# Kernel tuning notes

Measured on AMD Instinct MI355X. Metric: run time of the kernel, lower is better.

## Reference

```python
import jax, jax.numpy as jnp
import numpy as np

GRID_SIZE = 3
SPLINE_ORDER = 3

def make_grid():
    # grid_range=[-1,1], h=2/grid_size; extended grid of length grid_size+2k+1 = 10
    h = 2.0 / GRID_SIZE
    return (jnp.arange(-SPLINE_ORDER, GRID_SIZE + SPLINE_ORDER + 1, dtype=jnp.float32) * h - 1.0)

def b_splines(x, grid):
    # x: [N, F] -> bases [N, F, grid_size+spline_order]
    xg = x[..., None]
    bases = ((xg >= grid[:-1]) & (xg < grid[1:])).astype(x.dtype)
    for j in range(1, SPLINE_ORDER + 1):
        left = (xg - grid[: -(j + 1)]) / (grid[j:-1] - grid[: -(j + 1)])
        right = (grid[j + 1:] - xg) / (grid[j + 1:] - grid[1:-j])
        bases = left * bases[..., :-1] + right * bases[..., 1:]
    return bases

def kan_linear(x, base_w, spline_w, scaler, grid):
    # x: [N, F]; base_w: [O, F]; spline_w: [O, F, G]; scaler: [O, F]
    base = jax.nn.silu(x) @ base_w.T
    sb = b_splines(x, grid)                      # [N, F, G]
    spl = jnp.einsum('nfg,ofg->no', sb, spline_w * scaler[..., None])
    return base + spl

def kan_conv3x3(x, base_w, spline_w, scaler, grid):
    # x: [B, C, H, W]; 3x3 kernel, pad 1, stride 1 -> [B, O, H, W]
    B, C, H, W = x.shape
    patches = jax.lax.conv_general_dilated_patches(
        x, (3, 3), (1, 1), ((1, 1), (1, 1)))     # [B, C*9, H, W]
    p = patches.transpose(0, 2, 3, 1).reshape(B * H * W, C * 9)
    y = kan_linear(p, base_w, spline_w, scaler, grid)
    return y.reshape(B, H, W, -1).transpose(0, 3, 1, 2)

def maxpool2(x):
    return jax.lax.reduce_window(x, -jnp.inf, jax.lax.max,
                                 (1, 1, 2, 2), (1, 1, 2, 2), 'VALID')

def setup_inputs() -> dict:
    key = jax.random.key(0)
    ks = jax.random.split(key, 12)
    s = 0.1
    return {
        'x': jax.random.normal(ks[0], (256, 3, 32, 32), jnp.float32),
        'c1_base_w': jax.random.normal(ks[1], (8, 27), jnp.float32) * s,
        'c1_spline_w': jax.random.normal(ks[2], (8, 27, 6), jnp.float32) * s,
        'c1_scaler': jax.random.normal(ks[3], (8, 27), jnp.float32) * s,
        'c2_base_w': jax.random.normal(ks[4], (16, 72), jnp.float32) * s,
        'c2_spline_w': jax.random.normal(ks[5], (16, 72, 6), jnp.float32) * s,
        'c2_scaler': jax.random.normal(ks[6], (16, 72), jnp.float32) * s,
        'c3_base_w': jax.random.normal(ks[7], (32, 144), jnp.float32) * s,
        'c3_spline_w': jax.random.normal(ks[8], (32, 144, 6), jnp.float32) * s,
        'c3_scaler': jax.random.normal(ks[9], (32, 144), jnp.float32) * s,
        'lin_w': jax.random.normal(ks[10], (100, 512), jnp.float32) * s,
        'lin_b': jax.random.normal(ks[11], (100,), jnp.float32) * s,
    }

def reference(x, c1_base_w, c1_spline_w, c1_scaler,
              c2_base_w, c2_spline_w, c2_scaler,
              c3_base_w, c3_spline_w, c3_scaler,
              lin_w, lin_b):
    grid = make_grid()
    h = maxpool2(kan_conv3x3(x, c1_base_w, c1_spline_w, c1_scaler, grid))   # [B,8,16,16]
    h = maxpool2(kan_conv3x3(h, c2_base_w, c2_spline_w, c2_scaler, grid))   # [B,16,8,8]
    h = maxpool2(kan_conv3x3(h, c3_base_w, c3_spline_w, c3_scaler, grid))   # [B,32,4,4]
    h = h.reshape(h.shape[0], -1)                                           # [B,512]
    return h @ lin_w.T + lin_b                                              # [B,100]
```

## Files before the change

kernel.cpp:

```cpp
#include <hip/hip_runtime.h>
#include <hip/hip_bf16.h>
#include <math.h>


#define BATCH 256

typedef short bf16x8 __attribute__((ext_vector_type(8)));
typedef float f32x4  __attribute__((ext_vector_type(4)));

__device__ __forceinline__ unsigned pk2(float a, float b) {
    __hip_bfloat162 h = __float22bfloat162_rn(make_float2(a, b));
    unsigned u;
    __builtin_memcpy(&u, &h, 4);
    return u;
}
__device__ __forceinline__ unsigned f2bf(float f) {
    __hip_bfloat16 h = __float2bfloat16(f);
    unsigned short us;
    __builtin_memcpy(&us, &h, 2);
    return (unsigned)us;
}

__device__ __forceinline__ void bspline_basis(float x, float bs[6]) {
    float s  = (x + 3.0f) * 1.5f;
    float cf = floorf(s);
    float t  = s - cf;
    int  ci  = (int)cf;
    float t2 = t * t, t3 = t2 * t;
    float omt = 1.0f - t;
    const float k6 = 1.0f / 6.0f;
    float w0 = omt * omt * omt * k6;
    float w1 = (3.0f * t3 - 6.0f * t2 + 4.0f) * k6;
    float w2 = (-3.0f * t3 + 3.0f * t2 + 3.0f * t + 1.0f) * k6;
    float w3 = t3 * k6;
#pragma unroll
    for (int i = 0; i < 6; ++i) {
        int j = i - ci + 3;
        float v = 0.0f;
        v = (j == 0) ? w0 : v;
        v = (j == 1) ? w1 : v;
        v = (j == 2) ? w2 : v;
        v = (j == 3) ? w3 : v;
        bs[i] = v;
    }
}

__device__ __forceinline__ uint4 act_record(float val) {
    float silu = __fdividef(val, 1.0f + __expf(-val));
    float bs[6];
    bspline_basis(val, bs);
    uint4 r;
    r.x = pk2(silu, bs[0]);
    r.y = pk2(bs[1], bs[2]);
    r.z = pk2(bs[3], bs[4]);
    r.w = f2bf(bs[5]);
    return r;
}

__device__ __forceinline__ uint4 fuse_w(const float* bw, const float* sw,
                                        const float* sc, int j) {
    float s = sc[j];
    uint4 r;
    r.x = pk2(bw[j],             sw[j * 6 + 0] * s);
    r.y = pk2(sw[j * 6 + 1] * s, sw[j * 6 + 2] * s);
    r.z = pk2(sw[j * 6 + 3] * s, sw[j * 6 + 4] * s);
    r.w = f2bf(sw[j * 6 + 5] * s);
    return r;
}

__global__ __launch_bounds__(512, 4) void kan_l1(
        const float* __restrict__ x,
        const float* __restrict__ bw, const float* __restrict__ sw,
        const float* __restrict__ sc,
        const float* __restrict__ bw3, const float* __restrict__ sw3,
        const float* __restrict__ sc3,
        uint4* __restrict__ w3g,
        float* __restrict__ out) {
    constexpr int C = 3, F = 27, FP = 28, NS = 7;
    constexpr int RT = 18, TC = 34, NT = 512;

    __shared__ uint4 s_act[C * RT * TC];
    __shared__ uint4 s_w[FP * 16];

    const int tid = threadIdx.x;
    const int bid = blockIdx.x;
    const int b   = bid >> 1;
    const int v   = bid & 1;

    if (bid < 9) {
        int i = bid * NT + tid;
        if (i < 4608) {
            int o = i / 144, fp = i % 144;
            w3g[fp * 32 + o] = fuse_w(bw3, sw3, sc3, i);
        }
    }

    for (int i = tid; i < FP * 16; i += NT) {
        int fp = i >> 4, o = i & 15;
        uint4 r = make_uint4(0u, 0u, 0u, 0u);
        if (fp < F && o < 8) r = fuse_w(bw, sw, sc, o * F + fp);
        s_w[i] = r;
    }

    const uint4 zrec = act_record(0.0f);
    for (int i = tid; i < C * RT * TC; i += NT) s_act[i] = zrec;
    __syncthreads();
    const float* xb = x + (size_t)b * C * 32 * 32;
    if (tid < 408) {
        int cc  = tid / 136;
        int rem = tid - cc * 136;
        int rr_i = rem >> 3;
        int c4   = (rem & 7) * 4;
        float4 v4 = *(const float4*)&xb[(cc * 32 + rr_i + 15 * v) * 32 + c4];
        uint4* dst = &s_act[(cc * RT + rr_i + 1 - v) * TC + c4 + 1];
        dst[0] = act_record(v4.x);
        dst[1] = act_record(v4.y);
        dst[2] = act_record(v4.z);
        dst[3] = act_record(v4.w);
    }
    __syncthreads();

    const int lane = tid & 63;
    const int wv   = tid >> 6;
    const int kg   = lane >> 4;
    const int oc   = lane & 15;
    const int m    = lane & 15;

    bf16x8 bfr[NS];
#pragma unroll
    for (int s = 0; s < NS; ++s)
        bfr[s] = *reinterpret_cast<const bf16x8*>(&s_w[(4 * s + kg) * 16 + oc]);

    int pixoff[4];
#pragma unroll
    for (int t = 0; t < 4; ++t)
        pixoff[t] = (2 * wv + (t >> 1)) * TC + 16 * (t & 1) + m;

    f32x4 acc[4];
#pragma unroll
    for (int t = 0; t < 4; ++t) acc[t] = (f32x4){0.f, 0.f, 0.f, 0.f};

#pragma unroll
    for (int s = 0; s < NS; ++s) {
        int tp = 4 * s + kg;
        tp = (tp > F - 1) ? F - 1 : tp;
        int c  = tp / 9;
        int t9 = tp - 9 * c;
        int ky = t9 / 3;
        int kx = t9 - 3 * ky;
        int base = (c * RT + ky) * TC + kx;
#pragma unroll
        for (int t = 0; t < 4; ++t) {
            bf16x8 a = *reinterpret_cast<const bf16x8*>(&s_act[base + pixoff[t]]);
            acc[t] = __builtin_amdgcn_mfma_f32_16x16x32_bf16(a, bfr[s], acc[t], 0, 0, 0);
        }
    }

    if (oc < 8) {
        f32x4 e0, e1;
#pragma unroll
        for (int p = 0; p < 4; ++p) {
            e0[p] = fmaxf(acc[0][p], acc[2][p]);
            e1[p] = fmaxf(acc[1][p], acc[3][p]);
        }
        float* op = out + (((size_t)b * 8 + oc) * 16 + (8 * v + wv)) * 16;
        op[2 * kg]         = fmaxf(e0[0], e0[1]);
        op[2 * kg + 1]     = fmaxf(e0[2], e0[3]);
        op[8 + 2 * kg]     = fmaxf(e1[0], e1[1]);
        op[8 + 2 * kg + 1] = fmaxf(e1[2], e1[3]);
    }
}

__global__ __launch_bounds__(512, 2) void kan_l2l3lin(
        const float* __restrict__ h1,
        const float* __restrict__ bw2, const float* __restrict__ sw2,
        const float* __restrict__ sc2,
        const uint4* __restrict__ w3g,
        const float* __restrict__ lin_w, const float* __restrict__ lin_b,
        float* __restrict__ out) {
    constexpr int NT = 512;
    __shared__ alignas(16) unsigned char s_mem[59904];
    uint4* s_act2 = (uint4*)s_mem;
    uint4* s_w2   = (uint4*)(s_mem + 41472);
    float* s_h2   = (float*)s_mem;
    uint4* s_act3 = (uint4*)(s_mem + 4096);
    float* s_h3   = (float*)s_mem;

    const int tid = threadIdx.x;
    const int n   = blockIdx.x;
    const int lane = tid & 63;
    const int wv   = tid >> 6;
    const int kg   = lane >> 4;
    const int oc   = lane & 15;
    const int m    = lane & 15;

    const uint4 zrec = act_record(0.0f);

    for (int i = tid; i < 72 * 16; i += NT) {
        int fp = i >> 4, o = i & 15;
        s_w2[i] = fuse_w(bw2, sw2, sc2, o * 72 + fp);
    }
    for (int i = tid; i < 2592; i += NT) s_act2[i] = zrec;
    __syncthreads();
    {
        const float4* xb4 = (const float4*)(h1 + (size_t)n * 8 * 16 * 16);
        float4 v4 = xb4[tid];
        int cc   = tid >> 6;
        int rr_i = (tid >> 2) & 15;
        int c4   = (tid & 3) * 4;
        uint4* dst = &s_act2[(cc * 18 + rr_i + 1) * 18 + c4 + 1];
        dst[0] = act_record(v4.x);
        dst[1] = act_record(v4.y);
        dst[2] = act_record(v4.z);
        dst[3] = act_record(v4.w);
    }
    __syncthreads();

    {
        bf16x8 bfr2[18];
#pragma unroll
        for (int s = 0; s < 18; ++s)
            bfr2[s] = *reinterpret_cast<const bf16x8*>(&s_w2[(4 * s + kg) * 16 + oc]);
        const int p0 = (2 * wv) * 18 + m;
        const int p1 = p0 + 18;
        f32x4 a0 = (f32x4){0.f, 0.f, 0.f, 0.f}, a1 = a0, b0 = a0, b1 = a0;
#pragma unroll
        for (int s = 0; s < 18; ++s) {
            int tp = 4 * s + kg;
            int c  = tp / 9;
            int t9 = tp - 9 * c;
            int ky = t9 / 3;
            int kx = t9 - 3 * ky;
            int base = (c * 18 + ky) * 18 + kx;
            bf16x8 av0 = *reinterpret_cast<const bf16x8*>(&s_act2[base + p0]);
            bf16x8 av1 = *reinterpret_cast<const bf16x8*>(&s_act2[base + p1]);
            if (s < 9) {
                a0 = __builtin_amdgcn_mfma_f32_16x16x32_bf16(av0, bfr2[s], a0, 0, 0, 0);
                a1 = __builtin_amdgcn_mfma_f32_16x16x32_bf16(av1, bfr2[s], a1, 0, 0, 0);
            } else {
                b0 = __builtin_amdgcn_mfma_f32_16x16x32_bf16(av0, bfr2[s], b0, 0, 0, 0);
                b1 = __builtin_amdgcn_mfma_f32_16x16x32_bf16(av1, bfr2[s], b1, 0, 0, 0);
            }
        }
        a0 = a0 + b0;
        a1 = a1 + b1;
        float e0 = fmaxf(a0[0], a1[0]);
        float e1 = fmaxf(a0[1], a1[1]);
        float e2 = fmaxf(a0[2], a1[2]);
        float e3 = fmaxf(a0[3], a1[3]);
        __syncthreads();
        s_h2[(oc * 8 + wv) * 8 + 2 * kg]     = fmaxf(e0, e1);
        s_h2[(oc * 8 + wv) * 8 + 2 * kg + 1] = fmaxf(e2, e3);
    }
    __syncthreads();

    for (int i = tid; i < 1600; i += NT) s_act3[i] = zrec;
    __syncthreads();
    for (int i = tid; i < 1024; i += NT) {
        float val = s_h2[i];
        int cc   = i >> 6;
        int rr_i = (i >> 3) & 7;
        int col_i = i & 7;
        s_act3[(cc * 10 + rr_i + 1) * 10 + col_i + 1] = act_record(val);
    }
    __syncthreads();

    {
        const int mt  = wv & 3;
        const int o03 = 16 * (wv >> 2);
        bf16x8 bfr3[36];
#pragma unroll
        for (int s = 0; s < 36; ++s)
            bfr3[s] = *reinterpret_cast<const bf16x8*>(&w3g[(4 * s + kg) * 32 + o03 + oc]);
        const int poff = (2 * mt + (m >> 3)) * 10 + (m & 7);
        f32x4 a3 = (f32x4){0.f, 0.f, 0.f, 0.f}, a3b = a3;
#pragma unroll
        for (int s = 0; s < 36; ++s) {
            int tp = 4 * s + kg;
            int c  = tp / 9;
            int t9 = tp - 9 * c;
            int ky = t9 / 3;
            int kx = t9 - 3 * ky;
            int base = (c * 10 + ky) * 10 + kx;
            bf16x8 av = *reinterpret_cast<const bf16x8*>(&s_act3[base + poff]);
            if (s < 18)
                a3 = __builtin_amdgcn_mfma_f32_16x16x32_bf16(av, bfr3[s], a3, 0, 0, 0);
            else
                a3b = __builtin_amdgcn_mfma_f32_16x16x32_bf16(av, bfr3[s], a3b, 0, 0, 0);
        }
        a3 = a3 + a3b;
        float q0 = fmaxf(a3[0], a3[1]);
        float q1 = fmaxf(a3[2], a3[3]);
        float y0 = fmaxf(q0, __shfl_xor(q0, 32));
        float y1 = fmaxf(q1, __shfl_xor(q1, 32));
        if (kg < 2) {
            s_h3[(o03 + oc) * 16 + mt * 4 + 2 * kg]     = y0;
            s_h3[(o03 + oc) * 16 + mt * 4 + 2 * kg + 1] = y1;
        }
    }
    __syncthreads();

    {
        const float4* hf = (const float4*)s_h3;
        const float4 h0v = hf[lane];
        const float4 h1v = hf[lane + 64];
        const float4* wr = (const float4*)(lin_w + (size_t)wv * 512);
        float4 w0 = wr[lane];
        float4 w1 = wr[lane + 64];
#pragma unroll 1
        for (int o = wv; o < 100; o += 8) {
            float4 nw0, nw1;
            const int on = o + 8;
            if (on < 100) {
                const float4* wn = (const float4*)(lin_w + (size_t)on * 512);
                nw0 = wn[lane];
                nw1 = wn[lane + 64];
            }
            float p = w0.x * h0v.x + w0.y * h0v.y + w0.z * h0v.z + w0.w * h0v.w
                    + w1.x * h1v.x + w1.y * h1v.y + w1.z * h1v.z + w1.w * h1v.w;
            p += __shfl_xor(p, 32);
            p += __shfl_xor(p, 16);
            p += __shfl_xor(p, 8);
            p += __shfl_xor(p, 4);
            p += __shfl_xor(p, 2);
            p += __shfl_xor(p, 1);
            if (lane == 0) out[(size_t)n * 100 + o] = p + lin_b[o];
            w0 = nw0;
            w1 = nw1;
        }
    }
}

extern "C" void kernel_launch(void* const* d_in, const int* in_sizes, int n_in,
                              void* d_out, int out_size, void* d_ws, size_t ws_size,
                              hipStream_t stream) {
    const float* x     = (const float*)d_in[0];
    const float* c1_bw = (const float*)d_in[1];
    const float* c1_sw = (const float*)d_in[2];
    const float* c1_sc = (const float*)d_in[3];
    const float* c2_bw = (const float*)d_in[4];
    const float* c2_sw = (const float*)d_in[5];
    const float* c2_sc = (const float*)d_in[6];
    const float* c3_bw = (const float*)d_in[7];
    const float* c3_sw = (const float*)d_in[8];
    const float* c3_sc = (const float*)d_in[9];
    const float* lin_w = (const float*)d_in[10];
    const float* lin_b = (const float*)d_in[11];
    float* out = (float*)d_out;

    float* ws = (float*)d_ws;
    float* h1 = ws;
    uint4* w3g = (uint4*)(h1 + 524288);

    kan_l1<<<512, 512, 0, stream>>>(x, c1_bw, c1_sw, c1_sc,
                                    c3_bw, c3_sw, c3_sc, w3g, h1);
    kan_l2l3lin<<<256, 512, 0, stream>>>(h1, c2_bw, c2_sw, c2_sc,
                                         w3g, lin_w, lin_b, out);
}
```

Baseline: 98.91 us.

## Store layer-1 output as precomputed spline records and prefuse layer-2 weights globally

Layer 1 now writes its pooled outputs as packed bf16 activation/B-spline records instead of fp32 values, and also fuses layer-2 weights into a global buffer. Layer 2 copies records straight into shared memory and loads both layer-2 and layer-3 weight fragments into registers up front. This removes per-block basis evaluation and weight fusion in the second kernel and shrinks its shared memory. The cost is a fourfold larger intermediate tensor in global memory and higher register pressure from the hoisted weights.

```diff
diff --git a/kernel.cpp b/kernel.cpp
--- a/kernel.cpp
+++ b/kernel.cpp
@@ -72,10 +72,12 @@
         const float* __restrict__ x,
         const float* __restrict__ bw, const float* __restrict__ sw,
         const float* __restrict__ sc,
+        const float* __restrict__ bw2, const float* __restrict__ sw2,
+        const float* __restrict__ sc2,
         const float* __restrict__ bw3, const float* __restrict__ sw3,
         const float* __restrict__ sc3,
-        uint4* __restrict__ w3g,
-        float* __restrict__ out) {
+        uint4* __restrict__ w2g, uint4* __restrict__ w3g,
+        uint4* __restrict__ grec) {
     constexpr int C = 3, F = 27, FP = 28, NS = 7;
     constexpr int RT = 18, TC = 34, NT = 512;
 
@@ -87,11 +89,17 @@
     const int b   = bid >> 1;
     const int v   = bid & 1;
 
-    if (bid < 9) {
+    if (bid < 12) {
         int i = bid * NT + tid;
-        if (i < 4608) {
-            int o = i / 144, fp = i % 144;
-            w3g[fp * 32 + o] = fuse_w(bw3, sw3, sc3, i);
+        if (i < 5760) {
+            if (i < 1152) {
+                int o = i / 72, fp = i % 72;
+                w2g[fp * 16 + o] = fuse_w(bw2, sw2, sc2, i);
+            } else {
+                int j = i - 1152;
+                int o = j / 144, fp = j % 144;
+                w3g[fp * 32 + o] = fuse_w(bw3, sw3, sc3, j);
+            }
         }
     }
 
@@ -163,25 +171,23 @@
             e0[p] = fmaxf(acc[0][p], acc[2][p]);
             e1[p] = fmaxf(acc[1][p], acc[3][p]);
         }
-        float* op = out + (((size_t)b * 8 + oc) * 16 + (8 * v + wv)) * 16;
-        op[2 * kg]         = fmaxf(e0[0], e0[1]);
-        op[2 * kg + 1]     = fmaxf(e0[2], e0[3]);
-        op[8 + 2 * kg]     = fmaxf(e1[0], e1[1]);
-        op[8 + 2 * kg + 1] = fmaxf(e1[2], e1[3]);
+        uint4* op = grec + (((size_t)b * 8 + oc) * 16 + (8 * v + wv)) * 16;
+        op[2 * kg]         = act_record(fmaxf(e0[0], e0[1]));
+        op[2 * kg + 1]     = act_record(fmaxf(e0[2], e0[3]));
+        op[8 + 2 * kg]     = act_record(fmaxf(e1[0], e1[1]));
+        op[8 + 2 * kg + 1] = act_record(fmaxf(e1[2], e1[3]));
     }
 }
 
 __global__ __launch_bounds__(512, 2) void kan_l2l3lin(
-        const float* __restrict__ h1,
-        const float* __restrict__ bw2, const float* __restrict__ sw2,
-        const float* __restrict__ sc2,
+        const uint4* __restrict__ grec,
+        const uint4* __restrict__ w2g,
         const uint4* __restrict__ w3g,
         const float* __restrict__ lin_w, const float* __restrict__ lin_b,
         float* __restrict__ out) {
     constexpr int NT = 512;
-    __shared__ alignas(16) unsigned char s_mem[59904];
+    __shared__ alignas(16) unsigned char s_mem[41472];
     uint4* s_act2 = (uint4*)s_mem;
-    uint4* s_w2   = (uint4*)(s_mem + 41472);
     float* s_h2   = (float*)s_mem;
     uint4* s_act3 = (uint4*)(s_mem + 4096);
     float* s_h3   = (float*)s_mem;
@@ -196,31 +202,31 @@
 
     const uint4 zrec = act_record(0.0f);
 
-    for (int i = tid; i < 72 * 16; i += NT) {
-        int fp = i >> 4, o = i & 15;
-        s_w2[i] = fuse_w(bw2, sw2, sc2, o * 72 + fp);
-    }
+    bf16x8 bfr2[18];
+#pragma unroll
+    for (int s = 0; s < 18; ++s)
+        bfr2[s] = *reinterpret_cast<const bf16x8*>(&w2g[(4 * s + kg) * 16 + oc]);
+    const int o03 = 16 * (wv >> 2);
+    bf16x8 bfr3[36];
+#pragma unroll
+    for (int s = 0; s < 36; ++s)
+        bfr3[s] = *reinterpret_cast<const bf16x8*>(&w3g[(4 * s + kg) * 32 + o03 + oc]);
+
     for (int i = tid; i < 2592; i += NT) s_act2[i] = zrec;
     __syncthreads();
     {
-        const float4* xb4 = (const float4*)(h1 + (size_t)n * 8 * 16 * 16);
-        float4 v4 = xb4[tid];
-        int cc   = tid >> 6;
-        int rr_i = (tid >> 2) & 15;
-        int c4   = (tid & 3) * 4;
-        uint4* dst = &s_act2[(cc * 18 + rr_i + 1) * 18 + c4 + 1];
-        dst[0] = act_record(v4.x);
-        dst[1] = act_record(v4.y);
-        dst[2] = act_record(v4.z);
-        dst[3] = act_record(v4.w);
+        const uint4* grn = grec + (size_t)n * 2048;
+#pragma unroll
+        for (int k = 0; k < 4; ++k) {
+            int i = tid + k * NT;
+            uint4 r = grn[i];
+            int cc = i >> 8, rr_i = (i >> 4) & 15, col = i & 15;
+            s_act2[(cc * 18 + rr_i + 1) * 18 + col + 1] = r;
+        }
     }
     __syncthreads();
 
     {
-        bf16x8 bfr2[18];
-#pragma unroll
-        for (int s = 0; s < 18; ++s)
-            bfr2[s] = *reinterpret_cast<const bf16x8*>(&s_w2[(4 * s + kg) * 16 + oc]);
         const int p0 = (2 * wv) * 18 + m;
         const int p1 = p0 + 18;
         f32x4 a0 = (f32x4){0.f, 0.f, 0.f, 0.f}, a1 = a0, b0 = a0, b1 = a0;
@@ -267,11 +273,6 @@
 
     {
         const int mt  = wv & 3;
-        const int o03 = 16 * (wv >> 2);
-        bf16x8 bfr3[36];
-#pragma unroll
-        for (int s = 0; s < 36; ++s)
-            bfr3[s] = *reinterpret_cast<const bf16x8*>(&w3g[(4 * s + kg) * 32 + o03 + oc]);
         const int poff = (2 * mt + (m >> 3)) * 10 + (m & 7);
         f32x4 a3 = (f32x4){0.f, 0.f, 0.f, 0.f}, a3b = a3;
 #pragma unroll
@@ -348,12 +349,12 @@
     const float* lin_b = (const float*)d_in[11];
     float* out = (float*)d_out;
 
-    float* ws = (float*)d_ws;
-    float* h1 = ws;
-    uint4* w3g = (uint4*)(h1 + 524288);
+    uint4* grec = (uint4*)d_ws;
+    uint4* w2g  = grec + 524288;
+    uint4* w3g  = w2g + 1152;
 
     kan_l1<<<512, 512, 0, stream>>>(x, c1_bw, c1_sw, c1_sc,
-                                    c3_bw, c3_sw, c3_sc, w3g, h1);
-    kan_l2l3lin<<<256, 512, 0, stream>>>(h1, c2_bw, c2_sw, c2_sc,
-                                         w3g, lin_w, lin_b, out);
-}
+                                    c2_bw, c2_sw, c2_sc,
+                                    c3_bw, c3_sw, c3_sc, w2g, w3g, grec);
+    kan_l2l3lin<<<256, 512, 0, stream>>>(grec, w2g, w3g, lin_w, lin_b, out);
+}
```

Result: slower. 102.2 us (+3.3%).
